# Optimization experiments

Measured on AMD Instinct MI355X. Metric: run time of the kernel, lower is better.

Reference implementation:

```python
import jax, jax.numpy as jnp
import numpy as np

B, C, H, W = 8, 128, 64, 64
NWIN, HEADS, QKDIM, KVPW, TOPK = 8, 8, 128, 4, 16
SCALE = QKDIM ** -0.5

def _ln(x, g, b, eps):
    mu = x.mean(-1, keepdims=True)
    var = ((x - mu) ** 2).mean(-1, keepdims=True)
    return (x - mu) * jax.lax.rsqrt(var + eps) * g + b

def _conv(x, w, b, pad, groups=1):
    y = jax.lax.conv_general_dilated(x, w, (1, 1), [(pad, pad), (pad, pad)],
        dimension_numbers=('NCHW', 'OIHW', 'NCHW'), feature_group_count=groups)
    return y + b[None, :, None, None]

def setup_inputs():
    key = jax.random.key(0)
    ks = jax.random.split(key, 8)
    s = 0.05
    return {
        't1': jax.random.normal(ks[0], (B, C, H, W), jnp.float32),
        't2': jax.random.normal(ks[1], (B, C, H, W), jnp.float32),
        'pos_w': jax.random.normal(ks[2], (C, 1, 3, 3), jnp.float32) * s,
        'pos_b': jnp.zeros((C,), jnp.float32),
        'cat_w': jax.random.normal(ks[3], (C, 2 * C, 3, 3), jnp.float32) * s,
        'cat_b': jnp.zeros((C,), jnp.float32),
        'ln_cat_g': jnp.ones((C,), jnp.float32),
        'ln_cat_b': jnp.zeros((C,), jnp.float32),
        'ln1_g': jnp.ones((C,), jnp.float32),
        'ln1_b': jnp.zeros((C,), jnp.float32),
        'qkv_w': jax.random.normal(ks[4], (2 * QKDIM + C, C), jnp.float32) * s,
        'qkv_b': jnp.zeros((2 * QKDIM + C,), jnp.float32),
        'lepe_w': jax.random.normal(ks[5], (C, 1, 5, 5), jnp.float32) * s,
        'lepe_b': jnp.zeros((C,), jnp.float32),
        'wo_w': jax.random.normal(ks[6], (C, C), jnp.float32) * s,
        'wo_b': jnp.zeros((C,), jnp.float32),
    }

def _bra_cross(q_in, kv_in, qkv_w, qkv_b, lepe_w, lepe_b, wo_w, wo_b):
    # Bi-level routing cross attention: queries from q_in, keys/values from kv_in (NHWC).
    p = NWIN; wh, ww = H // p, W // p; p2 = p * p
    q = (q_in @ qkv_w.T + qkv_b)[..., :QKDIM]          # (B,H,W,QKDIM)
    kv = (kv_in @ qkv_w.T + qkv_b)[..., QKDIM:]        # (B,H,W,QKDIM+C)

    def win(x):
        c = x.shape[-1]
        return x.reshape(B, p, wh, p, ww, c).transpose(0, 1, 3, 2, 4, 5).reshape(B, p2, wh, ww, c)

    qw, kvw = win(q), win(kv)
    q_pix = qw.reshape(B, p2, wh * ww, QKDIM)
    # adaptive avg-pool each window's kv to KVPW x KVPW ('ada_avgpool')
    f = wh // KVPW
    kv_pix = kvw.reshape(B, p2, KVPW, f, KVPW, f, QKDIM + C).mean(axis=(3, 5))
    kv_pix = kv_pix.reshape(B, p2, KVPW * KVPW, QKDIM + C)
    q_win = qw.mean(axis=(2, 3))                        # (B,p2,QKDIM)
    k_win = kvw[..., :QKDIM].mean(axis=(2, 3))
    # LePE: depthwise 5x5 conv on full-resolution v
    v_full = kv[..., QKDIM:].transpose(0, 3, 1, 2)
    lepe = _conv(v_full, lepe_w, lepe_b, 2, groups=C).transpose(0, 2, 3, 1)
    # region-level routing (detached: diff_routing=False)
    logits = jnp.einsum('bpc,bqc->bpq',
                        jax.lax.stop_gradient(q_win) * SCALE,
                        jax.lax.stop_gradient(k_win))
    _, r_idx = jax.lax.top_k(logits, TOPK)              # (B,p2,TOPK)
    # gather kv of routed regions: (B,p2,TOPK,KVPW^2,QKDIM+C)
    kv_sel = jax.vmap(lambda kvp, idx: kvp[idx])(kv_pix, r_idx)
    k_sel = kv_sel[..., :QKDIM].reshape(B, p2, TOPK * KVPW * KVPW, HEADS, QKDIM // HEADS)
    v_sel = kv_sel[..., QKDIM:].reshape(B, p2, TOPK * KVPW * KVPW, HEADS, C // HEADS)
    q_h = q_pix.reshape(B, p2, wh * ww, HEADS, QKDIM // HEADS)
    attn = jnp.einsum('bpqmc,bpkmc->bpmqk', q_h * SCALE, k_sel)
    attn = jax.nn.softmax(attn, axis=-1)
    out = jnp.einsum('bpmqk,bpkmc->bpqmc', attn, v_sel).reshape(B, p2, wh, ww, C)
    out = out.reshape(B, p, p, wh, ww, C).transpose(0, 1, 3, 2, 4, 5).reshape(B, H, W, C)
    out = out + lepe
    return out @ wo_w.T + wo_b

def reference(t1, t2, pos_w, pos_b, cat_w, cat_b, ln_cat_g, ln_cat_b,
              ln1_g, ln1_b, qkv_w, qkv_b, lepe_w, lepe_b, wo_w, wo_b):
    # Block.forward: depthwise conv positional embedding
    t1 = t1 + _conv(t1, pos_w, pos_b, 1, groups=C)
    t2 = t2 + _conv(t2, pos_w, pos_b, 1, groups=C)
    t1n = t1.transpose(0, 2, 3, 1)
    t2n = t2.transpose(0, 2, 3, 1)
    # RGBConcatConv: cat on channel-last, 3x3 conv, relu(LayerNorm)
    xc = jnp.concatenate([t1n, t2n], axis=3).transpose(0, 3, 1, 2)
    xc = _conv(xc, cat_w, cat_b, 1).transpose(0, 2, 3, 1)
    x = jax.nn.relu(_ln(xc, ln_cat_g, ln_cat_b, 1e-5))
    attn = _bra_cross(_ln(t1n, ln1_g, ln1_b, 1e-6), _ln(t2n, ln1_g, ln1_b, 1e-6),
                      qkv_w, qkv_b, lepe_w, lepe_b, wo_w, wo_b)
    x = x + attn
    return x.transpose(0, 3, 1, 2)
```

## Files before the change

kernel.cpp:

```cpp
#include <hip/hip_runtime.h>
#include <math.h>

typedef unsigned short ushort_t;
typedef __attribute__((ext_vector_type(4))) float f32x4;
typedef __attribute__((ext_vector_type(16))) float f32x16;
typedef __attribute__((ext_vector_type(8))) short bf16x8;

constexpr int B = 8, C = 128, H = 64, W = 64;
constexpr int HEADS = 8, TOPK = 16;
constexpr int P2 = 64;
constexpr float SCALE = 0.0883883476483184405f;

constexpr size_t NPIX    = (size_t)B * H * W;
constexpr size_t OFF_T1C = 0;
constexpr size_t OFF_T2C = OFF_T1C + NPIX * 128;
constexpr size_t OFF_X   = OFF_T2C + NPIX * 128;
constexpr size_t OFF_QB  = OFF_X   + NPIX * 128;
constexpr size_t OFF_KV  = OFF_QB  + NPIX * 64;
constexpr size_t OFF_KVP = OFF_KV  + NPIX * 256;
constexpr size_t OFF_RW1 = OFF_KVP + 524288;
constexpr size_t OFF_RW2 = OFF_RW1 + 524288;
constexpr size_t OFF_KVPT= OFF_KVP + (size_t)B * P2 * 16 * 256;
constexpr size_t OFF_QW  = OFF_KVPT+ (size_t)B * P2 * 128 * 16 / 2;
constexpr size_t OFF_KW  = OFF_QW  + (size_t)B * P2 * 128;
constexpr size_t OFF_RIDX= OFF_KW  + (size_t)B * P2 * 128;
constexpr size_t OFF_WCB = OFF_RIDX+ (size_t)B * P2 * TOPK;
constexpr size_t OFF_QKVB= OFF_WCB + (size_t)9 * 256 * 128;
constexpr size_t OFF_WOB = OFF_QKVB+ (size_t)384 * 128 / 2;
constexpr size_t OFF_T1B = OFF_WOB + 8192;
constexpr size_t OFF_T2B = OFF_T1B + NPIX * 64;

__device__ inline ushort_t f2bf(float f) {
    unsigned u = __float_as_uint(f);
    unsigned r = u + 0x7FFFu + ((u >> 16) & 1u);
    return (ushort_t)(r >> 16);
}
__device__ inline float bf2f(ushort_t u) {
    return __uint_as_float((unsigned)u << 16);
}

__global__ __launch_bounds__(256) void prep_pos_k(
        const float* __restrict__ t1, const float* __restrict__ t2,
        const float* __restrict__ pos_w, const float* __restrict__ pos_b,
        const float* __restrict__ qkv_w, const float* __restrict__ wo_w,
        const float* __restrict__ cat_w,
        ushort_t* __restrict__ qkvB, ushort_t* __restrict__ woB,
        ushort_t* __restrict__ wcat2,
        float* __restrict__ out1, float* __restrict__ out2,
        ushort_t* __restrict__ ob1, ushort_t* __restrict__ ob2) {
    __shared__ float tile[4][32][33];
    int bid = blockIdx.x;
    int t = threadIdx.x;
    if (bid < 1152) {
        int idx = bid * 256 + t;
        if (idx < 384 * 128) qkvB[idx] = f2bf(qkv_w[idx]);
        if (idx < 128 * 128) woB[idx]  = f2bf(wo_w[idx]);
        if (idx < 36 * 8 * 128 * 8) {
            int i  = idx & 7;
            int n  = (idx >> 3) & 127;
            int r  = idx >> 10;
            int lg = r & 3;
            int kk = (r >> 2) & 1;
            int sdd = r >> 3;
            int dd = sdd % 9, q = sdd / 9;
            int ci = q * 64 + kk * 32 + lg * 8 + i;
            wcat2[idx] = f2bf(cat_w[((size_t)n * 256 + ci) * 9 + dd]);
        }
        return;
    }
    int pb = bid - 1152;
    int xb = pb & 1, cg = (pb >> 1) & 3, z = pb >> 3;
    int which = z >> 7, rem = z & 127;
    int b = rem >> 4, y0 = (rem & 15) * 4;
    const float* in = which ? t2 : t1;
    float* outNHWC = which ? out2 : out1;
    ushort_t* outB = which ? ob2 : ob1;
    int c0 = cg * 32, x0 = xb * 32;
    int tx = t & 31, tg = t >> 5;
    int x = x0 + tx;
    for (int i = 0; i < 4; i++) {
        int cl = tg * 4 + i, c = c0 + cl;
        const float* base = in + (size_t)(b * C + c) * H * W;
        float wv[9];
#pragma unroll
        for (int j = 0; j < 9; j++) wv[j] = pos_w[c * 9 + j];
        float rows[6][3];
#pragma unroll
        for (int yy = 0; yy < 6; yy++) {
            int gy = y0 - 1 + yy;
            bool yok = (gy >= 0 && gy < H);
#pragma unroll
            for (int dx = 0; dx < 3; dx++) {
                int gx = x + dx - 1;
                rows[yy][dx] = (yok && gx >= 0 && gx < W) ? base[gy * W + gx] : 0.f;
            }
        }
        float bb = pos_b[c];
#pragma unroll
        for (int k = 0; k < 4; k++) {
            float acc = rows[k + 1][1] + bb;
#pragma unroll
            for (int dy = 0; dy < 3; dy++)
#pragma unroll
                for (int dx = 0; dx < 3; dx++)
                    acc += rows[k + dy][dx] * wv[dy * 3 + dx];
            tile[k][cl][tx] = acc;
        }
    }
    __syncthreads();
    for (int k = 0; k < 4; k++)
        for (int i = 0; i < 4; i++) {
            int xl = tg * 4 + i;
            float val = tile[k][tx][xl];
            size_t idx = ((size_t)(b * H + y0 + k) * W + x0 + xl) * 128 + c0 + tx;
            outNHWC[idx] = val;
            outB[idx] = f2bf(val);
        }
}

__global__ __launch_bounds__(512) void cat_ln_k(
        const ushort_t* __restrict__ t1b, const ushort_t* __restrict__ t2b,
        const ushort_t* __restrict__ wcat2,
        const float* __restrict__ cat_b,
        const float* __restrict__ gcat, const float* __restrict__ bcat,
        ushort_t* __restrict__ xbuf,
        const float* __restrict__ t1c, const float* __restrict__ t2c,
        const float* __restrict__ g1, const float* __restrict__ b1,
        const ushort_t* __restrict__ qkvB, const float* __restrict__ qkv_b,
        ushort_t* __restrict__ outQ, ushort_t* __restrict__ outKV,
        float* __restrict__ rw1, float* __restrict__ rw2) {
    __shared__ __align__(16) unsigned char smem[64 * 272 * 2];
    int bid = blockIdx.x;
    int t = threadIdx.x;
    int lane = t & 63, wv = t >> 6;
    int l15 = lane & 15, lg = lane >> 4;

    if (bid < 512) {
        unsigned char* ash = smem;
        int which = bid >> 8;
        int blk = bid & 255;
        const float* in = which ? t2c : t1c;
        float* rw = which ? rw2 : rw1;
        size_t p0 = (size_t)blk * 128;
        int bb_ = blk >> 5, y0 = (blk & 31) * 2;
        {
            int row = t >> 2, sub = t & 3;
            const float* src = in + (p0 + row) * 128 + sub * 32;
            float4 v[8];
            float s = 0.f;
#pragma unroll
            for (int j = 0; j < 8; j++) {
                v[j] = *reinterpret_cast<const float4*>(src + j * 4);
                s += v[j].x + v[j].y + v[j].z + v[j].w;
            }
            s += __shfl_xor(s, 1, 64); s += __shfl_xor(s, 2, 64);
            float mean = s * (1.f / 128.f);
            float s2 = 0.f;
#pragma unroll
            for (int j = 0; j < 8; j++) {
                float dx = v[j].x - mean, dy = v[j].y - mean;
                float dz = v[j].z - mean, dw = v[j].w - mean;
                s2 += dx * dx + dy * dy + dz * dz + dw * dw;
            }
            s2 += __shfl_xor(s2, 1, 64); s2 += __shfl_xor(s2, 2, 64);
            float inv = rsqrtf(s2 * (1.f / 128.f) + 1e-6f);
            int wj = (wv & 3) * 2 + (lane >> 5);
            int yy_ = y0 + (wv >> 2);
            bool writer = (lane & 28) == 0;
            float* rwp = rw + (((size_t)(bb_ * 8 + wj) * 64 + yy_) * 128) + sub * 32;
#pragma unroll
            for (int j = 0; j < 8; j++) {
                int c = sub * 32 + j * 4;
                float4 gv = *reinterpret_cast<const float4*>(g1 + c);
                float4 bv = *reinterpret_cast<const float4*>(b1 + c);
                float o0 = (v[j].x - mean) * inv * gv.x + bv.x;
                float o1 = (v[j].y - mean) * inv * gv.y + bv.y;
                float o2 = (v[j].z - mean) * inv * gv.z + bv.z;
                float o3 = (v[j].w - mean) * inv * gv.w + bv.w;
                uint2 pk;
                pk.x = (unsigned)f2bf(o0) | ((unsigned)f2bf(o1) << 16);
                pk.y = (unsigned)f2bf(o2) | ((unsigned)f2bf(o3) << 16);
                *reinterpret_cast<uint2*>(ash + row * 272 + c * 2) = pk;
                float r0 = o0, r1 = o1, r2 = o2, r3 = o3;
#pragma unroll
                for (int m = 4; m <= 16; m <<= 1) {
                    r0 += __shfl_xor(r0, m, 64);
                    r1 += __shfl_xor(r1, m, 64);
                    r2 += __shfl_xor(r2, m, 64);
                    r3 += __shfl_xor(r3, m, 64);
                }
                if (writer)
                    *reinterpret_cast<float4*>(rwp + j * 4) = make_float4(r0, r1, r2, r3);
            }
        }
        __syncthreads();
        int mh = wv >> 2, nw = wv & 3;
        if (which == 0) {
            f32x4 acc[4][2];
#pragma unroll
            for (int mt = 0; mt < 4; mt++)
#pragma unroll
                for (int nn = 0; nn < 2; nn++)
                    acc[mt][nn] = (f32x4){0.f, 0.f, 0.f, 0.f};
#pragma unroll
            for (int ks = 0; ks < 4; ks++) {
                bf16x8 af[4];
#pragma unroll
                for (int mt = 0; mt < 4; mt++)
                    af[mt] = *reinterpret_cast<const bf16x8*>(
                        ash + (mh * 64 + mt * 16 + l15) * 272 + ks * 64 + lg * 16);
#pragma unroll
                for (int nn = 0; nn < 2; nn++) {
                    int n = (nw * 2 + nn) * 16 + l15;
                    bf16x8 bfr = *reinterpret_cast<const bf16x8*>(
                        qkvB + (size_t)n * 128 + ks * 32 + lg * 8);
#pragma unroll
                    for (int mt = 0; mt < 4; mt++)
                        acc[mt][nn] = __builtin_amdgcn_mfma_f32_16x16x32_bf16(
                            af[mt], bfr, acc[mt][nn], 0, 0, 0);
                }
            }
#pragma unroll
            for (int nn = 0; nn < 2; nn++) {
                int cg = (nw * 2 + nn) * 16 + l15;
                float bv = qkv_b[cg];
#pragma unroll
                for (int mt = 0; mt < 4; mt++)
#pragma unroll
                    for (int i = 0; i < 4; i++) {
                        size_t pix = p0 + mh * 64 + mt * 16 + lg * 4 + i;
                        outQ[pix * 128 + cg] = f2bf((acc[mt][nn][i] + bv) * SCALE);
                    }
            }
        } else {
            f32x4 acc[4][4];
#pragma unroll
            for (int mt = 0; mt < 4; mt++)
#pragma unroll
                for (int nn = 0; nn < 4; nn++)
                    acc[mt][nn] = (f32x4){0.f, 0.f, 0.f, 0.f};
#pragma unroll
            for (int ks = 0; ks < 4; ks++) {
                bf16x8 af[4];
#pragma unroll
                for (int mt = 0; mt < 4; mt++)
                    af[mt] = *reinterpret_cast<const bf16x8*>(
                        ash + (mh * 64 + mt * 16 + l15) * 272 + ks * 64 + lg * 16);
#pragma unroll
                for (int nn = 0; nn < 4; nn++) {
                    int n = 128 + (nw * 4 + nn) * 16 + l15;
                    bf16x8 bfr = *reinterpret_cast<const bf16x8*>(
                        qkvB + (size_t)n * 128 + ks * 32 + lg * 8);
#pragma unroll
                    for (int mt = 0; mt < 4; mt++)
                        acc[mt][nn] = __builtin_amdgcn_mfma_f32_16x16x32_bf16(
                            af[mt], bfr, acc[mt][nn], 0, 0, 0);
                }
            }
#pragma unroll
            for (int nn = 0; nn < 4; nn++) {
                int cg = (nw * 4 + nn) * 16 + l15;
                float bv = qkv_b[128 + cg];
#pragma unroll
                for (int mt = 0; mt < 4; mt++)
#pragma unroll
                    for (int i = 0; i < 4; i++) {
                        size_t pix = p0 + mh * 64 + mt * 16 + lg * 4 + i;
                        outKV[pix * 256 + cg] = f2bf(acc[mt][nn][i] + bv);
                    }
            }
        }
        return;
    }

    int cb = bid - 512;
    int mw = wv >> 2, nw = wv & 3;
    int b = cb >> 6, y0 = ((cb >> 3) & 7) * 8, x0 = (cb & 7) * 8;

    f32x4 acc[2][2];
#pragma unroll
    for (int m = 0; m < 2; m++)
#pragma unroll
        for (int cf = 0; cf < 2; cf++)
            acc[m][cf] = (f32x4){0.f, 0.f, 0.f, 0.f};

    int pyA[2], pxA[2];
#pragma unroll
    for (int m = 0; m < 2; m++) {
        int p = mw * 32 + m * 16 + l15;
        pyA[m] = p >> 3; pxA[m] = p & 7;
    }

    for (int q = 0; q < 4; q++) {
        __syncthreads();
        {
            const ushort_t* src = (q < 2 ? t1b : t2b);
            int coff = (q & 1) * 64;
            for (int e = t; e < 800; e += 512) {
                int pix = e >> 3, c8 = e & 7;
                int hy = pix / 10, hx = pix - hy * 10;
                int gy = y0 - 1 + hy, gx = x0 - 1 + hx;
                uint4 v = make_uint4(0u, 0u, 0u, 0u);
                if (gy >= 0 && gy < H && gx >= 0 && gx < W)
                    v = *reinterpret_cast<const uint4*>(
                        src + ((size_t)(b * H + gy) * W + gx) * 128 + coff + c8 * 8);
                *reinterpret_cast<uint4*>(smem + pix * 144 + c8 * 16) = v;
            }
        }
        __syncthreads();
#pragma unroll
        for (int dd = 0; dd < 9; dd++) {
            int dy = dd / 3, dx = dd - dy * 3;
            const ushort_t* wb = wcat2 + ((size_t)((q * 9 + dd) * 8 + lg) * 128) * 8;
            bf16x8 bfr[2][2];
#pragma unroll
            for (int kk = 0; kk < 2; kk++)
#pragma unroll
                for (int cf = 0; cf < 2; cf++)
                    bfr[kk][cf] = *reinterpret_cast<const bf16x8*>(
                        wb + (size_t)kk * 4096 + (nw * 32 + cf * 16 + l15) * 8);
            bf16x8 af[2][2];
#pragma unroll
            for (int m = 0; m < 2; m++)
#pragma unroll
                for (int kk = 0; kk < 2; kk++)
                    af[m][kk] = *reinterpret_cast<const bf16x8*>(
                        smem + ((pyA[m] + dy) * 10 + pxA[m] + dx) * 144 + kk * 64 + lg * 16);
#pragma unroll
            for (int m = 0; m < 2; m++)
#pragma unroll
                for (int cf = 0; cf < 2; cf++)
#pragma unroll
                    for (int kk = 0; kk < 2; kk++)
                        acc[m][cf] = __builtin_amdgcn_mfma_f32_16x16x32_bf16(
                            af[m][kk], bfr[kk][cf], acc[m][cf], 0, 0, 0);
        }
    }

    __syncthreads();
    float* res = (float*)smem;
    float* mstat = (float*)(smem + 64 * 132 * 4);
#pragma unroll
    for (int cf = 0; cf < 2; cf++) {
        int n = nw * 32 + cf * 16 + l15;
        float cbv = cat_b[n];
#pragma unroll
        for (int m = 0; m < 2; m++)
#pragma unroll
            for (int i = 0; i < 4; i++)
                res[(mw * 32 + m * 16 + lg * 4 + i) * 132 + n] = acc[m][cf][i] + cbv;
    }
    __syncthreads();
    {
        int pix = t >> 3, sub = t & 7;
        float s1 = 0.f;
#pragma unroll
        for (int j = 0; j < 16; j++) s1 += res[pix * 132 + sub + j * 8];
        s1 += __shfl_xor(s1, 1, 64);
        s1 += __shfl_xor(s1, 2, 64);
        s1 += __shfl_xor(s1, 4, 64);
        float mean = s1 * (1.f / 128.f);
        float s2 = 0.f;
#pragma unroll
        for (int j = 0; j < 16; j++) {
            float d = res[pix * 132 + sub + j * 8] - mean;
            s2 += d * d;
        }
        s2 += __shfl_xor(s2, 1, 64);
        s2 += __shfl_xor(s2, 2, 64);
        s2 += __shfl_xor(s2, 4, 64);
        float inv = rsqrtf(s2 * (1.f / 128.f) + 1e-5f);
        if (sub == 0) { mstat[pix] = mean; mstat[64 + pix] = inv; }
    }
    __syncthreads();
    {
        int c = t & 127, pg = t >> 7;
        float gg = gcat[c], bb = bcat[c];
        for (int j = 0; j < 16; j++) {
            int p2 = j * 4 + pg;
            float v = (res[p2 * 132 + c] - mstat[p2]) * mstat[64 + p2] * gg + bb;
            int py = p2 >> 3, px = p2 & 7;
            xbuf[((size_t)(b * H + y0 + py) * W + x0 + px) * 128 + c] = f2bf(fmaxf(v, 0.f));
        }
    }
}

__global__ __launch_bounds__(256) void route_pool_k(
        const float* __restrict__ rw1, const float* __restrict__ rw2,
        const float* __restrict__ qkv_w, const float* __restrict__ qkv_b,
        float* __restrict__ qwin, float* __restrict__ kwin,
        const ushort_t* __restrict__ kv,
        ushort_t* __restrict__ kb, ushort_t* __restrict__ kvpT,
        ushort_t* __restrict__ vpl) {
    __shared__ float msh[2][8][128];
    int bid = blockIdx.x;
    int t = threadIdx.x;
    if (bid < 64) {
        int b = bid >> 3, wi = bid & 7;
        for (int i = t; i < 8 * 128; i += 256) {
            int r = i >> 7, c = i & 127;
            size_t off = (((size_t)(b * 8 + r) * 64) + wi * 8) * 128 + c;
            float s1 = 0.f, s2 = 0.f;
#pragma unroll
            for (int rr = 0; rr < 8; rr++) {
                s1 += rw1[off + rr * 128];
                s2 += rw2[off + rr * 128];
            }
            msh[0][r][c] = s1 * (1.f / 64.f);
            msh[1][r][c] = s2 * (1.f / 64.f);
        }
        __syncthreads();
        int c = t;
        int which = c >> 7;
        const float* wrow = qkv_w + (size_t)c * 128;
        float acc[8];
#pragma unroll
        for (int r = 0; r < 8; r++) acc[r] = 0.f;
        for (int k = 0; k < 128; k++) {
            float wv_ = wrow[k];
#pragma unroll
            for (int r = 0; r < 8; r++) acc[r] += msh[which][r][k] * wv_;
        }
        float bv = qkv_b[c];
#pragma unroll
        for (int r = 0; r < 8; r++) {
            size_t o = ((size_t)b * 64 + wi * 8 + r) * 128 + (c & 127);
            (which ? kwin : qwin)[o] = acc[r] + bv;
        }
        return;
    }
    int pb = bid - 64;
    int b = pb >> 6, wdw = pb & 63;
    int wi = wdw >> 3, wj = wdw & 7;
    if (t < 128) {
        float vals[16];
        for (int ry = 0; ry < 4; ry++)
            for (int rx = 0; rx < 4; rx++) {
                float s = 0.f;
                for (int fy = 0; fy < 2; fy++)
                    for (int fx = 0; fx < 2; fx++) {
                        int y = wi * 8 + ry * 2 + fy, x = wj * 8 + rx * 2 + fx;
                        s += bf2f(kv[((size_t)(b * H + y) * W + x) * 256 + t]);
                    }
                vals[ry * 4 + rx] = s * 0.25f;
            }
#pragma unroll
        for (int pos = 0; pos < 16; pos++)
            kb[(((size_t)(b * 64 + wdw)) * 16 + pos) * 128 + t] = f2bf(vals[pos]);
    } else {
        int c = t - 128;
        float ps[4][4];
#pragma unroll
        for (int i = 0; i < 4; i++)
#pragma unroll
            for (int j = 0; j < 4; j++) ps[i][j] = 0.f;
        for (int y = 0; y < 8; y++) {
            union { ushort_t u16[8]; uint4 u4; } raw;
#pragma unroll
            for (int x = 0; x < 8; x++) {
                raw.u16[x] = kv[((size_t)(b * H + wi * 8 + y) * W + wj * 8 + x) * 256 + 128 + c];
                ps[y >> 1][x >> 1] += bf2f(raw.u16[x]);
            }
            *reinterpret_cast<uint4*>(
                vpl + ((size_t)(b * C + c) * H + wi * 8 + y) * W + wj * 8) = raw.u4;
        }
        union { ushort_t u16[16]; uint4 u4[2]; } pk;
#pragma unroll
        for (int ry = 0; ry < 4; ry++)
#pragma unroll
            for (int rx = 0; rx < 4; rx++)
                pk.u16[ry * 4 + rx] = f2bf(ps[ry][rx] * 0.25f);
        size_t base = (((size_t)(b * 64 + wdw)) * 128 + c) * 16;
        *reinterpret_cast<uint4*>(kvpT + base) = pk.u4[0];
        *reinterpret_cast<uint4*>(kvpT + base + 8) = pk.u4[1];
    }
}

__global__ __launch_bounds__(256) void route_lepe_k(
        const float* __restrict__ q_win, const float* __restrict__ k_win,
        int* __restrict__ r_idx,
        const ushort_t* __restrict__ vpl,
        const float* __restrict__ w, const float* __restrict__ bias,
        ushort_t* __restrict__ lep) {
    __shared__ float tile[68][69];
    int bid = blockIdx.x;
    int t = threadIdx.x;
    if (bid < 128) {
        int b = bid >> 4, p = (bid & 15) * 4 + (t >> 6);
        int j = t & 63;
        const float* qp = q_win + (size_t)(b * 64 + p) * 128;
        const float* kp = k_win + (size_t)(b * 64 + j) * 128;
        float lg = 0.f;
        for (int c = 0; c < 128; c++) lg += qp[c] * kp[c];
        lg *= SCALE;
        for (int it = 0; it < TOPK; it++) {
            float v = lg; int idx = j;
#pragma unroll
            for (int m = 32; m > 0; m >>= 1) {
                float ov = __shfl_xor(v, m, 64);
                int   oi = __shfl_xor(idx, m, 64);
                if (ov > v || (ov == v && oi < idx)) { v = ov; idx = oi; }
            }
            if (j == 0) r_idx[(size_t)(b * 64 + p) * TOPK + it] = idx;
            if (j == idx) lg = -__builtin_inff();
        }
        return;
    }
    int lb = bid - 128;
    int c = lb & 127, b = lb >> 7;
    const ushort_t* plane = vpl + (size_t)(b * C + c) * 4096;
    for (int e = t; e < 68 * 68; e += 256) {
        int row = e / 68, col = e - row * 68;
        int gy = row - 2, gx = col - 2;
        tile[row][col] = (gy >= 0 && gy < 64 && gx >= 0 && gx < 64)
                         ? bf2f(plane[gy * 64 + gx]) : 0.f;
    }
    float wv[25];
#pragma unroll
    for (int j = 0; j < 25; j++) wv[j] = w[c * 25 + j];
    float bb = bias[c];
    __syncthreads();
    int y = t >> 2, x0 = (t & 3) * 16;
    float acc[16];
#pragma unroll
    for (int i = 0; i < 16; i++) acc[i] = bb;
#pragma unroll
    for (int dy = 0; dy < 5; dy++) {
        float vals[20];
#pragma unroll
        for (int j = 0; j < 20; j++) vals[j] = tile[y + dy][x0 + j];
#pragma unroll
        for (int dx = 0; dx < 5; dx++)
#pragma unroll
            for (int i = 0; i < 16; i++)
                acc[i] += vals[i + dx] * wv[dy * 5 + dx];
    }
    ushort_t* dst = lep + (size_t)(b * C + c) * 4096 + y * 64 + x0;
    union { ushort_t u16[16]; uint4 u4[2]; } pk;
#pragma unroll
    for (int i = 0; i < 16; i++) pk.u16[i] = f2bf(acc[i]);
    *reinterpret_cast<uint4*>(dst) = pk.u4[0];
    *reinterpret_cast<uint4*>(dst + 8) = pk.u4[1];
}

__global__ __launch_bounds__(256) void attn_mfma_k(
        const ushort_t* __restrict__ qb,
        const ushort_t* __restrict__ kb,
        const ushort_t* __restrict__ kvpT,
        const int* __restrict__ r_idx,
        ushort_t* __restrict__ o) {
    __shared__ int ridx_sh[16];
    __shared__ float denom_sh[4][32];
    __shared__ __align__(16) ushort_t osh[64][32];

    int b = blockIdx.z, p = blockIdx.x, pair = blockIdx.y;
    int wi = p >> 3, wj = p & 7;
    int t = threadIdx.x;
    int lane = t & 63, wv = t >> 6;
    int l31 = lane & 31, hi = lane >> 5;

    if (t < 16) ridx_sh[t] = r_idx[(size_t)(b * 64 + p) * TOPK + t];
    __syncthreads();

    int hh = wv >> 1, qt = wv & 1;
    int h = pair * 2 + hh;

    int q = qt * 32 + l31;
    int qy = wi * 8 + (q >> 3), qx = wj * 8 + (q & 7);
    bf16x8 qf = *reinterpret_cast<const bf16x8*>(
        qb + ((size_t)(b * H + qy) * W + qx) * 128 + h * 16 + hi * 8);

    const ushort_t* kb_b = kb + (size_t)b * 64 * 16 * 128 + h * 16 + hi * 8;
    const ushort_t* vt_b = kvpT + (size_t)b * 64 * 128 * 16 + (h * 16 + (l31 & 15)) * 16 + hi * 8;

    float m_run = -INFINITY, l_run = 0.f;
    f32x16 opv;
#pragma unroll
    for (int r = 0; r < 16; r++) opv[r] = 0.f;
    f32x16 zf;
#pragma unroll
    for (int r = 0; r < 16; r++) zf[r] = 0.f;

    bf16x8 kf = *reinterpret_cast<const bf16x8*>(
        kb_b + ((size_t)ridx_sh[l31 >> 4] * 16 + (l31 & 15)) * 128);
    bf16x8 v0 = *reinterpret_cast<const bf16x8*>(vt_b + (size_t)ridx_sh[0] * 2048);
    bf16x8 v1 = *reinterpret_cast<const bf16x8*>(vt_b + (size_t)ridx_sh[1] * 2048);

    for (int t8 = 0; t8 < 8; t8++) {
        bf16x8 kfn = kf, v0n = v0, v1n = v1;
        if (t8 < 7) {
            kfn = *reinterpret_cast<const bf16x8*>(
                kb_b + ((size_t)ridx_sh[2 * t8 + 2 + (l31 >> 4)] * 16 + (l31 & 15)) * 128);
            v0n = *reinterpret_cast<const bf16x8*>(vt_b + (size_t)ridx_sh[2 * t8 + 2] * 2048);
            v1n = *reinterpret_cast<const bf16x8*>(vt_b + (size_t)ridx_sh[2 * t8 + 3] * 2048);
        }
        f32x16 S = __builtin_amdgcn_mfma_f32_32x32x16_bf16(kf, qf, zf, 0, 0, 0);
        float tm = S[0];
#pragma unroll
        for (int r = 1; r < 16; r++) tm = fmaxf(tm, S[r]);
        tm = fmaxf(tm, __shfl_xor(tm, 32, 64));
        float m_new = fmaxf(m_run, tm);
        float corr = __expf(m_run - m_new);
        float p_[16], psum = 0.f;
#pragma unroll
        for (int r = 0; r < 16; r++) { p_[r] = __expf(S[r] - m_new); psum += p_[r]; }
        psum += __shfl_xor(psum, 32, 64);
        l_run = l_run * corr + psum;
        m_run = m_new;
#pragma unroll
        for (int r = 0; r < 16; r++) opv[r] *= corr;
        unsigned w_[8], pw_[8];
#pragma unroll
        for (int j = 0; j < 8; j++)
            w_[j] = (__float_as_uint(p_[2 * j]) >> 16) |
                    (__float_as_uint(p_[2 * j + 1]) & 0xFFFF0000u);
#pragma unroll
        for (int j = 0; j < 8; j++) pw_[j] = __shfl_xor(w_[j], 32, 64);
        union { unsigned u[4]; bf16x8 v; } fa0, fa1;
        fa0.u[0] = hi ? pw_[2] : w_[0];
        fa0.u[1] = hi ? pw_[3] : w_[1];
        fa0.u[2] = hi ? w_[2]  : pw_[0];
        fa0.u[3] = hi ? w_[3]  : pw_[1];
        fa1.u[0] = hi ? pw_[6] : w_[4];
        fa1.u[1] = hi ? pw_[7] : w_[5];
        fa1.u[2] = hi ? w_[6]  : pw_[4];
        fa1.u[3] = hi ? w_[7]  : pw_[5];
        opv = __builtin_amdgcn_mfma_f32_32x32x16_bf16(fa0.v, v0, opv, 0, 0, 0);
        opv = __builtin_amdgcn_mfma_f32_32x32x16_bf16(fa1.v, v1, opv, 0, 0, 0);
        kf = kfn; v0 = v0n; v1 = v1n;
    }
    denom_sh[wv][l31] = l_run;
    if (l31 < 16) {
#pragma unroll
        for (int r = 0; r < 16; r++) {
            int qr = (r & 3) + 8 * (r >> 2) + 4 * hi;
            float invd = 1.f / denom_sh[wv][qr];
            osh[qt * 32 + qr][hh * 16 + l31] = f2bf(opv[r] * invd);
        }
    }
    __syncthreads();
    {
        int p_ = t >> 2, seg = t & 3;
        int y = wi * 8 + (p_ >> 3), x = wj * 8 + (p_ & 7);
        *reinterpret_cast<uint4*>(
            o + ((size_t)(b * H + y) * W + x) * 128 + pair * 32 + seg * 8) =
            *reinterpret_cast<const uint4*>(&osh[p_][seg * 8]);
    }
}

__global__ __launch_bounds__(256) void epilogue_mfma_k(
        const ushort_t* __restrict__ o,
        const ushort_t* __restrict__ lep,
        const ushort_t* __restrict__ xbuf,
        const ushort_t* __restrict__ woB,
        const float* __restrict__ wo_b,
        float* __restrict__ out) {
    __shared__ __align__(16) unsigned char smem[128 * 68 * 4];
    ushort_t* ash = (ushort_t*)smem;
    float* res = (float*)smem;
    int t = threadIdx.x, lane = t & 63, wv = t >> 6;
    int bid = blockIdx.x;
    int b = bid >> 6, y = bid & 63;
    size_t p0 = (size_t)bid * 64;

#pragma unroll
    for (int k = 0; k < 4; k++) {
        int e = k * 256 + t;
        int c = e >> 3, xg = e & 7;
        union { uint4 u4; ushort_t u16[8]; } v;
        v.u4 = *reinterpret_cast<const uint4*>(
            lep + (((size_t)(b * C + c) * 64 + y) * 64) + xg * 8);
#pragma unroll
        for (int j = 0; j < 8; j++) ash[(xg * 8 + j) * 136 + c] = v.u16[j];
    }
    __syncthreads();
    {
        int x = t >> 2, sub = t & 3;
        const ushort_t* op = o + (p0 + x) * 128 + sub * 32;
        ushort_t* ap = ash + x * 136 + sub * 32;
#pragma unroll
        for (int jj = 0; jj < 4; jj++) {
            union { uint4 u4; ushort_t u16[8]; } ov, lv;
            ov.u4 = *reinterpret_cast<const uint4*>(op + jj * 8);
            lv.u4 = *reinterpret_cast<const uint4*>(ap + jj * 8);
#pragma unroll
            for (int j = 0; j < 8; j++)
                lv.u16[j] = f2bf(bf2f(ov.u16[j]) + bf2f(lv.u16[j]));
            *reinterpret_cast<uint4*>(ap + jj * 8) = lv.u4;
        }
    }
    __syncthreads();
    int l15 = lane & 15, lg = lane >> 4;
    f32x4 acc[4][2];
#pragma unroll
    for (int mt = 0; mt < 4; mt++)
#pragma unroll
        for (int nn = 0; nn < 2; nn++)
            acc[mt][nn] = (f32x4){0.f, 0.f, 0.f, 0.f};
#pragma unroll
    for (int ks = 0; ks < 4; ks++) {
        bf16x8 af[4];
#pragma unroll
        for (int mt = 0; mt < 4; mt++)
            af[mt] = *reinterpret_cast<const bf16x8*>(
                ash + (mt * 16 + l15) * 136 + ks * 32 + lg * 8);
#pragma unroll
        for (int nn = 0; nn < 2; nn++) {
            int n = (wv * 2 + nn) * 16 + l15;
            bf16x8 bfr = *reinterpret_cast<const bf16x8*>(
                woB + (size_t)n * 128 + ks * 32 + lg * 8);
#pragma unroll
            for (int mt = 0; mt < 4; mt++)
                acc[mt][nn] = __builtin_amdgcn_mfma_f32_16x16x32_bf16(
                    af[mt], bfr, acc[mt][nn], 0, 0, 0);
        }
    }
    __syncthreads();
#pragma unroll
    for (int nn = 0; nn < 2; nn++) {
        int n = (wv * 2 + nn) * 16 + l15;
        float wb = wo_b[n];
#pragma unroll
        for (int mt = 0; mt < 4; mt++)
#pragma unroll
            for (int i = 0; i < 4; i++) {
                int r = mt * 16 + lg * 4 + i;
                float xb = bf2f(xbuf[(p0 + r) * 128 + n]);
                res[n * 68 + r] = acc[mt][nn][i] + wb + xb;
            }
    }
    __syncthreads();
    {
        int c = t >> 1, x0 = (t & 1) * 32;
        float* dst = out + ((size_t)(b * C + c) * 64 + y) * 64 + x0;
#pragma unroll
        for (int gblk = 0; gblk < 8; gblk++)
            *reinterpret_cast<float4*>(dst + gblk * 4) =
                *reinterpret_cast<const float4*>(&res[c * 68 + x0 + gblk * 4]);
    }
}

extern "C" void kernel_launch(void* const* d_in, const int* in_sizes, int n_in,
                              void* d_out, int out_size, void* d_ws, size_t ws_size,
                              hipStream_t stream) {
    const float* t1      = (const float*)d_in[0];
    const float* t2      = (const float*)d_in[1];
    const float* pos_w   = (const float*)d_in[2];
    const float* pos_b   = (const float*)d_in[3];
    const float* cat_w   = (const float*)d_in[4];
    const float* cat_b   = (const float*)d_in[5];
    const float* ln_cat_g= (const float*)d_in[6];
    const float* ln_cat_b= (const float*)d_in[7];
    const float* ln1_g   = (const float*)d_in[8];
    const float* ln1_b   = (const float*)d_in[9];
    const float* qkv_w   = (const float*)d_in[10];
    const float* qkv_b   = (const float*)d_in[11];
    const float* lepe_w  = (const float*)d_in[12];
    const float* lepe_b  = (const float*)d_in[13];
    const float* wo_w    = (const float*)d_in[14];
    const float* wo_b    = (const float*)d_in[15];

    float* ws    = (float*)d_ws;
    float* t1c   = ws + OFF_T1C;
    float* t2c   = ws + OFF_T2C;
    ushort_t* xbuf = (ushort_t*)(ws + OFF_X);
    ushort_t* qbuf = (ushort_t*)(ws + OFF_QB);
    ushort_t* kvbuf= (ushort_t*)(ws + OFF_KV);
    ushort_t* kb   = (ushort_t*)(ws + OFF_KVP);
    float* rw1   = ws + OFF_RW1;
    float* rw2   = ws + OFF_RW2;
    ushort_t* kvpT = (ushort_t*)(ws + OFF_KVPT);
    float* qwin  = ws + OFF_QW;
    float* kwin  = ws + OFF_KW;
    int*   ridx  = (int*)(ws + OFF_RIDX);
    ushort_t* wcat2 = (ushort_t*)(ws + OFF_WCB);
    ushort_t* qkvB  = (ushort_t*)(ws + OFF_QKVB);
    ushort_t* woB   = (ushort_t*)(ws + OFF_WOB);
    ushort_t* t1b   = (ushort_t*)(ws + OFF_T1B);
    ushort_t* t2b   = (ushort_t*)(ws + OFF_T2B);
    ushort_t* obuf  = (ushort_t*)(ws + OFF_T1C);
    ushort_t* vpl   = (ushort_t*)(ws + OFF_T2C);
    ushort_t* lep   = (ushort_t*)(ws + OFF_KV);
    float* out   = (float*)d_out;

    prep_pos_k<<<3200, 256, 0, stream>>>(
        t1, t2, pos_w, pos_b, qkv_w, wo_w, cat_w,
        qkvB, woB, wcat2, t1c, t2c, t1b, t2b);
    cat_ln_k<<<1024, 512, 0, stream>>>(
        t1b, t2b, wcat2, cat_b, ln_cat_g, ln_cat_b, xbuf,
        t1c, t2c, ln1_g, ln1_b, qkvB, qkv_b, qbuf, kvbuf, rw1, rw2);
    route_pool_k<<<576, 256, 0, stream>>>(
        rw1, rw2, qkv_w, qkv_b, qwin, kwin, kvbuf, kb, kvpT, vpl);
    route_lepe_k<<<1152, 256, 0, stream>>>(
        qwin, kwin, ridx, vpl, lepe_w, lepe_b, lep);
    attn_mfma_k<<<dim3(64, 4, B), 256, 0, stream>>>(qbuf, kb, kvpT, ridx, obuf);
    epilogue_mfma_k<<<512, 256, 0, stream>>>(obuf, lep, xbuf, woB, wo_b, out);
}
```

Measured before the change: 157.8 us.

## Reorder fused kernel blocks and compute conv LayerNorm stats in registers

Block indices in the fused kernel are swapped so the heavier 3x3 concat-conv blocks are scheduled first and the LN+QKV projection blocks follow. The conv epilogue now computes LayerNorm mean and variance from MFMA accumulators with shuffles and a small shared partial-sum buffer, instead of spilling the full fp32 tile to shared memory and rereading it. Output is staged as bf16 in shared memory and written with 16-byte vector stores. The single-pass E[x^2]-mean^2 variance is slightly less numerically robust than the old two-pass form.

New measurement: 164.6 us. 4.3% more time.

```diff
diff --git a/kernel.cpp b/kernel.cpp
--- a/kernel.cpp
+++ b/kernel.cpp
@@ -136,251 +136,261 @@
     int l15 = lane & 15, lg = lane >> 4;
 
     if (bid < 512) {
-        unsigned char* ash = smem;
-        int which = bid >> 8;
-        int blk = bid & 255;
-        const float* in = which ? t2c : t1c;
-        float* rw = which ? rw2 : rw1;
-        size_t p0 = (size_t)blk * 128;
-        int bb_ = blk >> 5, y0 = (blk & 31) * 2;
-        {
-            int row = t >> 2, sub = t & 3;
-            const float* src = in + (p0 + row) * 128 + sub * 32;
-            float4 v[8];
-            float s = 0.f;
-#pragma unroll
-            for (int j = 0; j < 8; j++) {
-                v[j] = *reinterpret_cast<const float4*>(src + j * 4);
-                s += v[j].x + v[j].y + v[j].z + v[j].w;
-            }
-            s += __shfl_xor(s, 1, 64); s += __shfl_xor(s, 2, 64);
-            float mean = s * (1.f / 128.f);
-            float s2 = 0.f;
-#pragma unroll
-            for (int j = 0; j < 8; j++) {
-                float dx = v[j].x - mean, dy = v[j].y - mean;
-                float dz = v[j].z - mean, dw = v[j].w - mean;
-                s2 += dx * dx + dy * dy + dz * dz + dw * dw;
-            }
-            s2 += __shfl_xor(s2, 1, 64); s2 += __shfl_xor(s2, 2, 64);
-            float inv = rsqrtf(s2 * (1.f / 128.f) + 1e-6f);
-            int wj = (wv & 3) * 2 + (lane >> 5);
-            int yy_ = y0 + (wv >> 2);
-            bool writer = (lane & 28) == 0;
-            float* rwp = rw + (((size_t)(bb_ * 8 + wj) * 64 + yy_) * 128) + sub * 32;
-#pragma unroll
-            for (int j = 0; j < 8; j++) {
-                int c = sub * 32 + j * 4;
-                float4 gv = *reinterpret_cast<const float4*>(g1 + c);
-                float4 bv = *reinterpret_cast<const float4*>(b1 + c);
-                float o0 = (v[j].x - mean) * inv * gv.x + bv.x;
-                float o1 = (v[j].y - mean) * inv * gv.y + bv.y;
-                float o2 = (v[j].z - mean) * inv * gv.z + bv.z;
-                float o3 = (v[j].w - mean) * inv * gv.w + bv.w;
-                uint2 pk;
-                pk.x = (unsigned)f2bf(o0) | ((unsigned)f2bf(o1) << 16);
-                pk.y = (unsigned)f2bf(o2) | ((unsigned)f2bf(o3) << 16);
-                *reinterpret_cast<uint2*>(ash + row * 272 + c * 2) = pk;
-                float r0 = o0, r1 = o1, r2 = o2, r3 = o3;
-#pragma unroll
-                for (int m = 4; m <= 16; m <<= 1) {
-                    r0 += __shfl_xor(r0, m, 64);
-                    r1 += __shfl_xor(r1, m, 64);
-                    r2 += __shfl_xor(r2, m, 64);
-                    r3 += __shfl_xor(r3, m, 64);
+        int cb = bid;
+        int mw = wv >> 2, nw = wv & 3;
+        int b = cb >> 6, y0 = ((cb >> 3) & 7) * 8, x0 = (cb & 7) * 8;
+
+        f32x4 acc[2][2];
+#pragma unroll
+        for (int m = 0; m < 2; m++)
+#pragma unroll
+            for (int cf = 0; cf < 2; cf++)
+                acc[m][cf] = (f32x4){0.f, 0.f, 0.f, 0.f};
+
+        int pyA[2], pxA[2];
+#pragma unroll
+        for (int m = 0; m < 2; m++) {
+            int p = mw * 32 + m * 16 + l15;
+            pyA[m] = p >> 3; pxA[m] = p & 7;
+        }
+
+        for (int q = 0; q < 4; q++) {
+            __syncthreads();
+            {
+                const ushort_t* src = (q < 2 ? t1b : t2b);
+                int coff = (q & 1) * 64;
+                for (int e = t; e < 800; e += 512) {
+                    int pix = e >> 3, c8 = e & 7;
+                    int hy = pix / 10, hx = pix - hy * 10;
+                    int gy = y0 - 1 + hy, gx = x0 - 1 + hx;
+                    uint4 v = make_uint4(0u, 0u, 0u, 0u);
+                    if (gy >= 0 && gy < H && gx >= 0 && gx < W)
+                        v = *reinterpret_cast<const uint4*>(
+                            src + ((size_t)(b * H + gy) * W + gx) * 128 + coff + c8 * 8);
+                    *reinterpret_cast<uint4*>(smem + pix * 144 + c8 * 16) = v;
                 }
-                if (writer)
-                    *reinterpret_cast<float4*>(rwp + j * 4) = make_float4(r0, r1, r2, r3);
-            }
-        }
+            }
+            __syncthreads();
+#pragma unroll
+            for (int dd = 0; dd < 9; dd++) {
+                int dy = dd / 3, dx = dd - dy * 3;
+                const ushort_t* wb = wcat2 + ((size_t)((q * 9 + dd) * 8 + lg) * 128) * 8;
+                bf16x8 bfr[2][2];
+#pragma unroll
+                for (int kk = 0; kk < 2; kk++)
+#pragma unroll
+                    for (int cf = 0; cf < 2; cf++)
+                        bfr[kk][cf] = *reinterpret_cast<const bf16x8*>(
+                            wb + (size_t)kk * 4096 + (nw * 32 + cf * 16 + l15) * 8);
+                bf16x8 af[2][2];
+#pragma unroll
+                for (int m = 0; m < 2; m++)
+#pragma unroll
+                    for (int kk = 0; kk < 2; kk++)
+                        af[m][kk] = *reinterpret_cast<const bf16x8*>(
+                            smem + ((pyA[m] + dy) * 10 + pxA[m] + dx) * 144 + kk * 64 + lg * 16);
+#pragma unroll
+                for (int m = 0; m < 2; m++)
+#pragma unroll
+                    for (int cf = 0; cf < 2; cf++)
+#pragma unroll
+                        for (int kk = 0; kk < 2; kk++)
+                            acc[m][cf] = __builtin_amdgcn_mfma_f32_16x16x32_bf16(
+                                af[m][kk], bfr[kk][cf], acc[m][cf], 0, 0, 0);
+            }
+        }
+
+        ushort_t* xsh = (ushort_t*)smem;
+        float* psum  = (float*)(smem + 17408);
+        float* psum2 = (float*)(smem + 17408 + 2048);
+        float gv[2], bvv[2];
+#pragma unroll
+        for (int cf = 0; cf < 2; cf++) {
+            int n = nw * 32 + cf * 16 + l15;
+            float cbv = cat_b[n];
+            gv[cf] = gcat[n]; bvv[cf] = bcat[n];
+#pragma unroll
+            for (int m = 0; m < 2; m++)
+#pragma unroll
+                for (int i = 0; i < 4; i++) acc[m][cf][i] += cbv;
+        }
+#pragma unroll
+        for (int m = 0; m < 2; m++)
+#pragma unroll
+            for (int i = 0; i < 4; i++) {
+                float s = acc[m][0][i] + acc[m][1][i];
+                float s2 = acc[m][0][i] * acc[m][0][i] + acc[m][1][i] * acc[m][1][i];
+                s  += __shfl_xor(s, 1, 64);  s2 += __shfl_xor(s2, 1, 64);
+                s  += __shfl_xor(s, 2, 64);  s2 += __shfl_xor(s2, 2, 64);
+                s  += __shfl_xor(s, 4, 64);  s2 += __shfl_xor(s2, 4, 64);
+                s  += __shfl_xor(s, 8, 64);  s2 += __shfl_xor(s2, 8, 64);
+                int p = mw * 32 + m * 16 + lg * 4 + i;
+                if (l15 == 0) { psum[wv * 64 + p] = s; psum2[wv * 64 + p] = s2; }
+            }
         __syncthreads();
-        int mh = wv >> 2, nw = wv & 3;
-        if (which == 0) {
-            f32x4 acc[4][2];
+#pragma unroll
+        for (int m = 0; m < 2; m++)
+#pragma unroll
+            for (int i = 0; i < 4; i++) {
+                int p = mw * 32 + m * 16 + lg * 4 + i;
+                float tot = 0.f, tot2 = 0.f;
+#pragma unroll
+                for (int j = 0; j < 4; j++) {
+                    tot  += psum[(mw * 4 + j) * 64 + p];
+                    tot2 += psum2[(mw * 4 + j) * 64 + p];
+                }
+                float mean = tot * (1.f / 128.f);
+                float inv = rsqrtf(tot2 * (1.f / 128.f) - mean * mean + 1e-5f);
+#pragma unroll
+                for (int cf = 0; cf < 2; cf++) {
+                    float v = (acc[m][cf][i] - mean) * inv * gv[cf] + bvv[cf];
+                    xsh[p * 136 + nw * 32 + cf * 16 + l15] = f2bf(fmaxf(v, 0.f));
+                }
+            }
+        __syncthreads();
+        for (int e = t; e < 1024; e += 512) {
+            int pix = e >> 4, c16 = e & 15;
+            int gy = y0 + (pix >> 3), gx = x0 + (pix & 7);
+            *reinterpret_cast<uint4*>(
+                xbuf + ((size_t)(b * H + gy) * W + gx) * 128 + c16 * 8) =
+                *reinterpret_cast<const uint4*>(xsh + pix * 136 + c16 * 8);
+        }
+        return;
+    }
+
+    unsigned char* ash = smem;
+    int lb = bid - 512;
+    int which = lb >> 8;
+    int blk = lb & 255;
+    const float* in = which ? t2c : t1c;
+    float* rw = which ? rw2 : rw1;
+    size_t p0 = (size_t)blk * 128;
+    int bb_ = blk >> 5, y0 = (blk & 31) * 2;
+    {
+        int row = t >> 2, sub = t & 3;
+        const float* src = in + (p0 + row) * 128 + sub * 32;
+        float4 v[8];
+        float s = 0.f;
+#pragma unroll
+        for (int j = 0; j < 8; j++) {
+            v[j] = *reinterpret_cast<const float4*>(src + j * 4);
+            s += v[j].x + v[j].y + v[j].z + v[j].w;
+        }
+        s += __shfl_xor(s, 1, 64); s += __shfl_xor(s, 2, 64);
+        float mean = s * (1.f / 128.f);
+        float s2 = 0.f;
+#pragma unroll
+        for (int j = 0; j < 8; j++) {
+            float dx = v[j].x - mean, dy = v[j].y - mean;
+            float dz = v[j].z - mean, dw = v[j].w - mean;
+            s2 += dx * dx + dy * dy + dz * dz + dw * dw;
+        }
+        s2 += __shfl_xor(s2, 1, 64); s2 += __shfl_xor(s2, 2, 64);
+        float inv = rsqrtf(s2 * (1.f / 128.f) + 1e-6f);
+        int wj = (wv & 3) * 2 + (lane >> 5);
+        int yy_ = y0 + (wv >> 2);
+        bool writer = (lane & 28) == 0;
+        float* rwp = rw + (((size_t)(bb_ * 8 + wj) * 64 + yy_) * 128) + sub * 32;
+#pragma unroll
+        for (int j = 0; j < 8; j++) {
+            int c = sub * 32 + j * 4;
+            float4 gv = *reinterpret_cast<const float4*>(g1 + c);
+            float4 bv = *reinterpret_cast<const float4*>(b1 + c);
+            float o0 = (v[j].x - mean) * inv * gv.x + bv.x;
+            float o1 = (v[j].y - mean) * inv * gv.y + bv.y;
+            float o2 = (v[j].z - mean) * inv * gv.z + bv.z;
+            float o3 = (v[j].w - mean) * inv * gv.w + bv.w;
+            uint2 pk;
+            pk.x = (unsigned)f2bf(o0) | ((unsigned)f2bf(o1) << 16);
+            pk.y = (unsigned)f2bf(o2) | ((unsigned)f2bf(o3) << 16);
+            *reinterpret_cast<uint2*>(ash + row * 272 + c * 2) = pk;
+            float r0 = o0, r1 = o1, r2 = o2, r3 = o3;
+#pragma unroll
+            for (int m = 4; m <= 16; m <<= 1) {
+                r0 += __shfl_xor(r0, m, 64);
+                r1 += __shfl_xor(r1, m, 64);
+                r2 += __shfl_xor(r2, m, 64);
+                r3 += __shfl_xor(r3, m, 64);
+            }
+            if (writer)
+                *reinterpret_cast<float4*>(rwp + j * 4) = make_float4(r0, r1, r2, r3);
+        }
+    }
+    __syncthreads();
+    int mh = wv >> 2, nw = wv & 3;
+    if (which == 0) {
+        f32x4 acc[4][2];
+#pragma unroll
+        for (int mt = 0; mt < 4; mt++)
+#pragma unroll
+            for (int nn = 0; nn < 2; nn++)
+                acc[mt][nn] = (f32x4){0.f, 0.f, 0.f, 0.f};
+#pragma unroll
+        for (int ks = 0; ks < 4; ks++) {
+            bf16x8 af[4];
 #pragma unroll
             for (int mt = 0; mt < 4; mt++)
-#pragma unroll
-                for (int nn = 0; nn < 2; nn++)
-                    acc[mt][nn] = (f32x4){0.f, 0.f, 0.f, 0.f};
-#pragma unroll
-            for (int ks = 0; ks < 4; ks++) {
-                bf16x8 af[4];
+                af[mt] = *reinterpret_cast<const bf16x8*>(
+                    ash + (mh * 64 + mt * 16 + l15) * 272 + ks * 64 + lg * 16);
+#pragma unroll
+            for (int nn = 0; nn < 2; nn++) {
+                int n = (nw * 2 + nn) * 16 + l15;
+                bf16x8 bfr = *reinterpret_cast<const bf16x8*>(
+                    qkvB + (size_t)n * 128 + ks * 32 + lg * 8);
 #pragma unroll
                 for (int mt = 0; mt < 4; mt++)
-                    af[mt] = *reinterpret_cast<const bf16x8*>(
-                        ash + (mh * 64 + mt * 16 + l15) * 272 + ks * 64 + lg * 16);
-#pragma unroll
-                for (int nn = 0; nn < 2; nn++) {
-                    int n = (nw * 2 + nn) * 16 + l15;
-                    bf16x8 bfr = *reinterpret_cast<const bf16x8*>(
-                        qkvB + (size_t)n * 128 + ks * 32 + lg * 8);
-#pragma unroll
-                    for (int mt = 0; mt < 4; mt++)
-                        acc[mt][nn] = __builtin_amdgcn_mfma_f32_16x16x32_bf16(
-                            af[mt], bfr, acc[mt][nn], 0, 0, 0);
+                    acc[mt][nn] = __builtin_amdgcn_mfma_f32_16x16x32_bf16(
+                        af[mt], bfr, acc[mt][nn], 0, 0, 0);
+            }
+        }
+#pragma unroll
+        for (int nn = 0; nn < 2; nn++) {
+            int cg = (nw * 2 + nn) * 16 + l15;
+            float bv = qkv_b[cg];
+#pragma unroll
+            for (int mt = 0; mt < 4; mt++)
+#pragma unroll
+                for (int i = 0; i < 4; i++) {
+                    size_t pix = p0 + mh * 64 + mt * 16 + lg * 4 + i;
+                    outQ[pix * 128 + cg] = f2bf((acc[mt][nn][i] + bv) * SCALE);
                 }
-            }
-#pragma unroll
-            for (int nn = 0; nn < 2; nn++) {
-                int cg = (nw * 2 + nn) * 16 + l15;
-                float bv = qkv_b[cg];
+        }
+    } else {
+        f32x4 acc[4][4];
+#pragma unroll
+        for (int mt = 0; mt < 4; mt++)
+#pragma unroll
+            for (int nn = 0; nn < 4; nn++)
+                acc[mt][nn] = (f32x4){0.f, 0.f, 0.f, 0.f};
+#pragma unroll
+        for (int ks = 0; ks < 4; ks++) {
+            bf16x8 af[4];
+#pragma unroll
+            for (int mt = 0; mt < 4; mt++)
+                af[mt] = *reinterpret_cast<const bf16x8*>(
+                    ash + (mh * 64 + mt * 16 + l15) * 272 + ks * 64 + lg * 16);
+#pragma unroll
+            for (int nn = 0; nn < 4; nn++) {
+                int n = 128 + (nw * 4 + nn) * 16 + l15;
+                bf16x8 bfr = *reinterpret_cast<const bf16x8*>(
+                    qkvB + (size_t)n * 128 + ks * 32 + lg * 8);
 #pragma unroll
                 for (int mt = 0; mt < 4; mt++)
-#pragma unroll
-                    for (int i = 0; i < 4; i++) {
-                        size_t pix = p0 + mh * 64 + mt * 16 + lg * 4 + i;
-                        outQ[pix * 128 + cg] = f2bf((acc[mt][nn][i] + bv) * SCALE);
-                    }
-            }
-        } else {
-            f32x4 acc[4][4];
+                    acc[mt][nn] = __builtin_amdgcn_mfma_f32_16x16x32_bf16(
+                        af[mt], bfr, acc[mt][nn], 0, 0, 0);
+            }
+        }
+#pragma unroll
+        for (int nn = 0; nn < 4; nn++) {
+            int cg = (nw * 4 + nn) * 16 + l15;
+            float bv = qkv_b[128 + cg];
 #pragma unroll
             for (int mt = 0; mt < 4; mt++)
 #pragma unroll
-                for (int nn = 0; nn < 4; nn++)
-                    acc[mt][nn] = (f32x4){0.f, 0.f, 0.f, 0.f};
-#pragma unroll
-            for (int ks = 0; ks < 4; ks++) {
-                bf16x8 af[4];
-#pragma unroll
-                for (int mt = 0; mt < 4; mt++)
-                    af[mt] = *reinterpret_cast<const bf16x8*>(
-                        ash + (mh * 64 + mt * 16 + l15) * 272 + ks * 64 + lg * 16);
-#pragma unroll
-                for (int nn = 0; nn < 4; nn++) {
-                    int n = 128 + (nw * 4 + nn) * 16 + l15;
-                    bf16x8 bfr = *reinterpret_cast<const bf16x8*>(
-                        qkvB + (size_t)n * 128 + ks * 32 + lg * 8);
-#pragma unroll
-                    for (int mt = 0; mt < 4; mt++)
-                        acc[mt][nn] = __builtin_amdgcn_mfma_f32_16x16x32_bf16(
-                            af[mt], bfr, acc[mt][nn], 0, 0, 0);
+                for (int i = 0; i < 4; i++) {
+                    size_t pix = p0 + mh * 64 + mt * 16 + lg * 4 + i;
+                    outKV[pix * 256 + cg] = f2bf(acc[mt][nn][i] + bv);
                 }
-            }
-#pragma unroll
-            for (int nn = 0; nn < 4; nn++) {
-                int cg = (nw * 4 + nn) * 16 + l15;
-                float bv = qkv_b[128 + cg];
-#pragma unroll
-                for (int mt = 0; mt < 4; mt++)
-#pragma unroll
-                    for (int i = 0; i < 4; i++) {
-                        size_t pix = p0 + mh * 64 + mt * 16 + lg * 4 + i;
-                        outKV[pix * 256 + cg] = f2bf(acc[mt][nn][i] + bv);
-                    }
-            }
-        }
-        return;
-    }
-
-    int cb = bid - 512;
-    int mw = wv >> 2, nw = wv & 3;
-    int b = cb >> 6, y0 = ((cb >> 3) & 7) * 8, x0 = (cb & 7) * 8;
-
-    f32x4 acc[2][2];
-#pragma unroll
-    for (int m = 0; m < 2; m++)
-#pragma unroll
-        for (int cf = 0; cf < 2; cf++)
-            acc[m][cf] = (f32x4){0.f, 0.f, 0.f, 0.f};
-
-    int pyA[2], pxA[2];
-#pragma unroll
-    for (int m = 0; m < 2; m++) {
-        int p = mw * 32 + m * 16 + l15;
-        pyA[m] = p >> 3; pxA[m] = p & 7;
-    }
-
-    for (int q = 0; q < 4; q++) {
-        __syncthreads();
-        {
-            const ushort_t* src = (q < 2 ? t1b : t2b);
-            int coff = (q & 1) * 64;
-            for (int e = t; e < 800; e += 512) {
-                int pix = e >> 3, c8 = e & 7;
-                int hy = pix / 10, hx = pix - hy * 10;
-                int gy = y0 - 1 + hy, gx = x0 - 1 + hx;
-                uint4 v = make_uint4(0u, 0u, 0u, 0u);
-                if (gy >= 0 && gy < H && gx >= 0 && gx < W)
-                    v = *reinterpret_cast<const uint4*>(
-                        src + ((size_t)(b * H + gy) * W + gx) * 128 + coff + c8 * 8);
-                *reinterpret_cast<uint4*>(smem + pix * 144 + c8 * 16) = v;
-            }
-        }
-        __syncthreads();
-#pragma unroll
-        for (int dd = 0; dd < 9; dd++) {
-            int dy = dd / 3, dx = dd - dy * 3;
-            const ushort_t* wb = wcat2 + ((size_t)((q * 9 + dd) * 8 + lg) * 128) * 8;
-            bf16x8 bfr[2][2];
-#pragma unroll
-            for (int kk = 0; kk < 2; kk++)
-#pragma unroll
-                for (int cf = 0; cf < 2; cf++)
-                    bfr[kk][cf] = *reinterpret_cast<const bf16x8*>(
-                        wb + (size_t)kk * 4096 + (nw * 32 + cf * 16 + l15) * 8);
-            bf16x8 af[2][2];
-#pragma unroll
-            for (int m = 0; m < 2; m++)
-#pragma unroll
-                for (int kk = 0; kk < 2; kk++)
-                    af[m][kk] = *reinterpret_cast<const bf16x8*>(
-                        smem + ((pyA[m] + dy) * 10 + pxA[m] + dx) * 144 + kk * 64 + lg * 16);
-#pragma unroll
-            for (int m = 0; m < 2; m++)
-#pragma unroll
-                for (int cf = 0; cf < 2; cf++)
-#pragma unroll
-                    for (int kk = 0; kk < 2; kk++)
-                        acc[m][cf] = __builtin_amdgcn_mfma_f32_16x16x32_bf16(
-                            af[m][kk], bfr[kk][cf], acc[m][cf], 0, 0, 0);
-        }
-    }
-
-    __syncthreads();
-    float* res = (float*)smem;
-    float* mstat = (float*)(smem + 64 * 132 * 4);
-#pragma unroll
-    for (int cf = 0; cf < 2; cf++) {
-        int n = nw * 32 + cf * 16 + l15;
-        float cbv = cat_b[n];
-#pragma unroll
-        for (int m = 0; m < 2; m++)
-#pragma unroll
-            for (int i = 0; i < 4; i++)
-                res[(mw * 32 + m * 16 + lg * 4 + i) * 132 + n] = acc[m][cf][i] + cbv;
-    }
-    __syncthreads();
-    {
-        int pix = t >> 3, sub = t & 7;
-        float s1 = 0.f;
-#pragma unroll
-        for (int j = 0; j < 16; j++) s1 += res[pix * 132 + sub + j * 8];
-        s1 += __shfl_xor(s1, 1, 64);
-        s1 += __shfl_xor(s1, 2, 64);
-        s1 += __shfl_xor(s1, 4, 64);
-        float mean = s1 * (1.f / 128.f);
-        float s2 = 0.f;
-#pragma unroll
-        for (int j = 0; j < 16; j++) {
-            float d = res[pix * 132 + sub + j * 8] - mean;
-            s2 += d * d;
-        }
-        s2 += __shfl_xor(s2, 1, 64);
-        s2 += __shfl_xor(s2, 2, 64);
-        s2 += __shfl_xor(s2, 4, 64);
-        float inv = rsqrtf(s2 * (1.f / 128.f) + 1e-5f);
-        if (sub == 0) { mstat[pix] = mean; mstat[64 + pix] = inv; }
-    }
-    __syncthreads();
-    {
-        int c = t & 127, pg = t >> 7;
-        float gg = gcat[c], bb = bcat[c];
-        for (int j = 0; j < 16; j++) {
-            int p2 = j * 4 + pg;
-            float v = (res[p2 * 132 + c] - mstat[p2]) * mstat[64 + p2] * gg + bb;
-            int py = p2 >> 3, px = p2 & 7;
-            xbuf[((size_t)(b * H + y0 + py) * W + x0 + px) * 128 + c] = f2bf(fmaxf(v, 0.f));
         }
     }
 }
```
